# Performance work log

Hardware: AMD Instinct MI355X
Metric: run time of the kernel (lower is better)

## Reference

```python
import jax, jax.numpy as jnp
import numpy as np

NUM_CHANNELS = 256
NUM_HEADS = 4
HEAD_DIM = 64


def setup_inputs() -> dict:
    key = jax.random.key(0)
    k1, k2, k3, k4, k5 = jax.random.split(key, 5)
    C, H, D = NUM_CHANNELS, NUM_HEADS, HEAD_DIM
    x = jax.random.normal(k1, (8, C, 32, 32), dtype=jnp.float32)
    # projection: Linear(C -> H*D*3); stored as (in, out)
    Wp = jax.random.normal(k2, (C, H * D * 3), dtype=jnp.float32) / np.sqrt(C)
    bp = jnp.zeros((H * D * 3,), dtype=jnp.float32)
    # output: Linear(H*D -> C)
    Wo = jax.random.normal(k3, (H * D, C), dtype=jnp.float32) / np.sqrt(H * D)
    bo = jnp.zeros((C,), dtype=jnp.float32)
    return {"x": x, "Wp": Wp, "bp": bp, "Wo": Wo, "bo": bo}


def reference(x, Wp, bp, Wo, bo):
    B, C, Hh, Ww = x.shape
    Nh, Dh = NUM_HEADS, HEAD_DIM
    scale = Dh ** (-0.5)
    # (B, C, H, W) -> (B, N, C)
    xs = x.reshape(B, C, Hh * Ww).transpose(0, 2, 1)
    # QKV projection -> (B, N, heads, 3*head_dim)
    qkv = (xs @ Wp + bp).reshape(B, -1, Nh, 3 * Dh)
    q, k, v = jnp.split(qkv, 3, axis=-1)  # each (B, N, heads, head_dim)
    # NOTE: original forward never applies self.norm, so no GroupNorm here.
    attn = jnp.einsum('bihd,bjhd->bijh', q, k) * scale  # (B, N, N, heads)
    attn = jax.nn.softmax(attn, axis=2)
    res = jnp.einsum('bijh,bjhd->bihd', attn, v)  # (B, N, heads, head_dim)
    res = res.reshape(B, -1, Nh * Dh)
    res = res @ Wo + bo  # (B, N, C)
    out = res + xs
    return out.transpose(0, 2, 1).reshape(B, C, Hh, Ww)
```

## Files before the change

kernel.cpp:

```cpp
#include <hip/hip_runtime.h>

typedef __attribute__((ext_vector_type(8))) short short8;
typedef __attribute__((ext_vector_type(4))) float f32x4;

#define NB 8
#define NC 256
#define NH 4
#define ND 64
#define NN 1024
#define OC3 768

__device__ __forceinline__ unsigned short f2bf(float f) {
  union { float f; unsigned int u; } a;
  a.f = f;
  unsigned int r = a.u + 0x7fffu + ((a.u >> 16) & 1u);
  return (unsigned short)(r >> 16);
}

__device__ __forceinline__ unsigned int pkbf(float lo, float hi) {
  union { float f; unsigned int u; } a, b;
  a.f = lo; b.f = hi;
  return __builtin_amdgcn_perm(b.u + 0x8000u, a.u + 0x8000u, 0x07060302u);
}

typedef const unsigned int __attribute__((address_space(1)))* gp_t;
typedef unsigned int __attribute__((address_space(3)))* lp_t;
__device__ __forceinline__ void glds16(const unsigned short* g, unsigned short* l) {
  __builtin_amdgcn_global_load_lds((gp_t)g, (lp_t)l, 16, 0, 0);
}

__global__ __launch_bounds__(256) void trans_all(
    const float* __restrict__ x, const float* __restrict__ Wp,
    const float* __restrict__ Wo, unsigned short* __restrict__ xs,
    unsigned short* __restrict__ WpT, unsigned short* __restrict__ WoT) {
  __shared__ float T[64][65];
  int z = blockIdx.z;
  const float* in; unsigned short* out; int R, S;
  if (z < 8) { in = x + (size_t)z * NC * NN; out = xs + (size_t)z * NC * NN; R = NC; S = NN; }
  else if (z == 8) { if (blockIdx.x >= 12) return; in = Wp; out = WpT; R = NC; S = OC3; }
  else { if (blockIdx.x >= 4) return; in = Wo; out = WoT; R = NC; S = NC; }
  int s0 = blockIdx.x * 64, r0 = blockIdx.y * 64;
  int t = threadIdx.x;
  {
    int ri = t >> 2, sb = t & 3;
    const float* p = in + (size_t)(r0 + ri) * S + s0 + sb * 16;
    float4 v0 = *(const float4*)(p);
    float4 v1 = *(const float4*)(p + 4);
    float4 v2 = *(const float4*)(p + 8);
    float4 v3 = *(const float4*)(p + 12);
    float vv[16] = {v0.x, v0.y, v0.z, v0.w, v1.x, v1.y, v1.z, v1.w,
                    v2.x, v2.y, v2.z, v2.w, v3.x, v3.y, v3.z, v3.w};
#pragma unroll
    for (int e = 0; e < 16; ++e) T[ri][sb * 16 + e] = vv[e];
  }
  __syncthreads();
  {
    int so = t >> 2, rb = t & 3;
    union { unsigned short us[16]; uint4 v[2]; } pk;
#pragma unroll
    for (int e = 0; e < 16; ++e) pk.us[e] = f2bf(T[rb * 16 + e][so]);
    uint4* dst = (uint4*)(out + (size_t)(s0 + so) * R + r0 + rb * 16);
    dst[0] = pk.v[0];
    dst[1] = pk.v[1];
  }
}

__global__ __launch_bounds__(256) void gemm_qkv(
    const unsigned short* __restrict__ xs, const unsigned short* __restrict__ WpT,
    const float* __restrict__ bp,
    unsigned short* __restrict__ Qf, unsigned short* __restrict__ Kf,
    unsigned short* __restrict__ Vf) {
  __shared__ __attribute__((aligned(16))) unsigned short Al[64 * 72];
  __shared__ __attribute__((aligned(16))) unsigned short Bl[64 * 72];
  int nt = blockIdx.x, mt = blockIdx.y;
  int t = threadIdx.x, w = t >> 6, l = t & 63, q = l >> 4, c = l & 15;
  f32x4 acc[4] = {{0, 0, 0, 0}, {0, 0, 0, 0}, {0, 0, 0, 0}, {0, 0, 0, 0}};
  const unsigned short* Arow = xs + (size_t)(mt * 64) * NC;
  const unsigned short* Brow = WpT + (size_t)(nt * 64) * NC;
  for (int k0 = 0; k0 < NC; k0 += 64) {
    __syncthreads();
#pragma unroll
    for (int it = 0; it < 2; ++it) {
      int u = t + it * 256;
      int row = u >> 3, kb = u & 7;
      *(uint4*)&Al[row * 72 + kb * 8] = *(const uint4*)(Arow + (size_t)row * NC + k0 + kb * 8);
      *(uint4*)&Bl[row * 72 + kb * 8] = *(const uint4*)(Brow + (size_t)row * NC + k0 + kb * 8);
    }
    __syncthreads();
#pragma unroll
    for (int ks = 0; ks < 2; ++ks) {
      short8 a = *(const short8*)&Al[(w * 16 + c) * 72 + ks * 32 + q * 8];
#pragma unroll
      for (int ct = 0; ct < 4; ++ct) {
        short8 b = *(const short8*)&Bl[(ct * 16 + c) * 72 + ks * 32 + q * 8];
        acc[ct] = __builtin_amdgcn_mfma_f32_16x16x32_bf16(a, b, acc[ct], 0, 0, 0);
      }
    }
  }
  int o0 = nt * 64;
  int h = o0 / 192, rem = o0 % 192;
  int b = mt >> 4, itl = mt & 15;
  int bh = b * NH + h;
  size_t rbase = (size_t)bh * 65536;
#pragma unroll
  for (int ct = 0; ct < 4; ++ct) {
    float bias = bp[o0 + ct * 16 + c];
#pragma unroll
    for (int r = 0; r < 4; ++r) acc[ct][r] += bias;
  }
  if (rem < 128) {
    unsigned short* dst = (rem == 0) ? Qf : Kf;
    float sc = (rem == 0) ? 0.18033688011112042f : 1.0f;
#pragma unroll
    for (int ct = 0; ct < 4; ++ct) {
      int ks = ct >> 1, qf = (ct & 1) * 2 + (c >> 3), e = c & 7;
      size_t fbase = (rem == 0)
          ? rbase + (size_t)((itl * 4 + w) * 2 + ks) * 512
          : rbase + (size_t)(itl * 8 + ks * 4 + w) * 512;
      size_t off = fbase + (size_t)(qf * 16) * 8 + e;
#pragma unroll
      for (int r = 0; r < 4; ++r)
        dst[off + (q * 4 + r) * 8] = f2bf(acc[ct][r] * sc);
    }
  } else {
    int kv = w >> 1, ql = (w & 1) * 2 + (q >> 1);
#pragma unroll
    for (int ct = 0; ct < 4; ++ct) {
      size_t fbase = rbase + (size_t)(itl * 8 + kv * 4 + ct) * 512 + (ql * 16 + c) * 8
                   + (q & 1) * 4;
      uint2 pk2 = {pkbf(acc[ct][0], acc[ct][1]), pkbf(acc[ct][2], acc[ct][3])};
      *(uint2*)&Vf[fbase] = pk2;
    }
  }
}

__global__ __launch_bounds__(256) void attn(
    const unsigned short* __restrict__ Qf, const unsigned short* __restrict__ Kf,
    const unsigned short* __restrict__ Vf, unsigned short* __restrict__ O) {
  __shared__ __attribute__((aligned(16))) unsigned short Kl[2][4096];
  __shared__ __attribute__((aligned(16))) unsigned short Vl[2][4096];
  __shared__ __attribute__((aligned(16))) unsigned short Pl[4][1024];
  int B = blockIdx.x;
  int bh = (B & 7) + 8 * ((B >> 3) & 3);
  int it = B >> 5;
  int t = threadIdx.x, w = t >> 6, l = t & 63, q = l >> 4, c = l & 15;
  const unsigned short* Qt = Qf + (size_t)bh * 65536 + (size_t)(it * 4 + w) * 1024;
  short8 bq0 = *(const short8*)(Qt + l * 8);
  short8 bq1 = *(const short8*)(Qt + 512 + l * 8);
  const unsigned short* Kt = Kf + (size_t)bh * 65536;
  const unsigned short* Vt = Vf + (size_t)bh * 65536;

#pragma unroll
  for (int m = 0; m < 2; ++m) {
    int ch = (m * 4 + w) * 512;
    glds16(Kt + ch + l * 8, &Kl[0][ch]);
    glds16(Vt + ch + l * 8, &Vl[0][ch]);
  }

  float lsum = 0.f;
  f32x4 oacc[4] = {{0, 0, 0, 0}, {0, 0, 0, 0}, {0, 0, 0, 0}, {0, 0, 0, 0}};
  unsigned short* Pw = &Pl[w][0];
  int p = 0;
  for (int jt = 0; jt < 16; ++jt) {
    __syncthreads();
    if (jt < 15) {
      const unsigned short* ksn = Kt + (size_t)(jt + 1) * 4096;
      const unsigned short* vsn = Vt + (size_t)(jt + 1) * 4096;
#pragma unroll
      for (int m = 0; m < 2; ++m) {
        int ch = (m * 4 + w) * 512;
        glds16(ksn + ch + l * 8, &Kl[p ^ 1][ch]);
        glds16(vsn + ch + l * 8, &Vl[p ^ 1][ch]);
      }
    }
    f32x4 sT[4] = {{0, 0, 0, 0}, {0, 0, 0, 0}, {0, 0, 0, 0}, {0, 0, 0, 0}};
#pragma unroll
    for (int ks = 0; ks < 2; ++ks) {
      short8 bq = ks ? bq1 : bq0;
#pragma unroll
      for (int js = 0; js < 4; ++js) {
        short8 ka = *(const short8*)&Kl[p][(ks * 4 + js) * 512 + l * 8];
        sT[js] = __builtin_amdgcn_mfma_f32_16x16x32_bf16(ka, bq, sT[js], 0, 0, 0);
      }
    }
#pragma unroll
    for (int js = 0; js < 4; ++js) {
      float e0 = __builtin_amdgcn_exp2f(sT[js][0]);
      float e1 = __builtin_amdgcn_exp2f(sT[js][1]);
      float e2 = __builtin_amdgcn_exp2f(sT[js][2]);
      float e3 = __builtin_amdgcn_exp2f(sT[js][3]);
      lsum += (e0 + e1) + (e2 + e3);
      int base = (js >> 1) * 512 + (((js & 1) * 2 + (q >> 1)) * 16 + c) * 8 + (q & 1) * 4;
      *(unsigned int*)&Pw[base] = pkbf(e0, e1);
      *(unsigned int*)&Pw[base + 2] = pkbf(e2, e3);
    }
#pragma unroll
    for (int kv = 0; kv < 2; ++kv) {
      short8 pa = *(const short8*)&Pw[kv * 512 + l * 8];
#pragma unroll
      for (int dt = 0; dt < 4; ++dt) {
        short8 vv = *(const short8*)&Vl[p][(kv * 4 + dt) * 512 + l * 8];
        oacc[dt] = __builtin_amdgcn_mfma_f32_16x16x32_bf16(pa, vv, oacc[dt], 0, 0, 0);
      }
    }
    p ^= 1;
  }
  lsum += __shfl_xor(lsum, 16);
  lsum += __shfl_xor(lsum, 32);
  float invr[4];
#pragma unroll
  for (int r = 0; r < 4; ++r) invr[r] = 1.0f / __shfl(lsum, q * 4 + r, 64);
  int b = bh >> 2, h = bh & 3;
#pragma unroll
  for (int dt = 0; dt < 4; ++dt)
#pragma unroll
    for (int r = 0; r < 4; ++r) {
      int i = it * 64 + w * 16 + q * 4 + r;
      O[((size_t)b * NN + i) * NC + h * ND + dt * 16 + c] = f2bf(oacc[dt][r] * invr[r]);
    }
}

__global__ __launch_bounds__(256) void gemm_out(
    const unsigned short* __restrict__ O, const unsigned short* __restrict__ WoT,
    const float* __restrict__ bo, const float* __restrict__ x,
    float* __restrict__ out) {
  __shared__ __attribute__((aligned(16))) unsigned short Al[64 * 72];
  __shared__ __attribute__((aligned(16))) unsigned short Bl[64 * 72];
  __shared__ float Tl[64 * 65];
  int nt = blockIdx.x, mt = blockIdx.y;
  int t = threadIdx.x, w = t >> 6, l = t & 63, q = l >> 4, c = l & 15;
  f32x4 acc[4] = {{0, 0, 0, 0}, {0, 0, 0, 0}, {0, 0, 0, 0}, {0, 0, 0, 0}};
  const unsigned short* Arow = O + (size_t)(mt * 64) * NC;
  const unsigned short* Brow = WoT + (size_t)(nt * 64) * NC;
  for (int k0 = 0; k0 < NC; k0 += 64) {
    __syncthreads();
#pragma unroll
    for (int it = 0; it < 2; ++it) {
      int u = t + it * 256;
      int row = u >> 3, kb = u & 7;
      *(uint4*)&Al[row * 72 + kb * 8] = *(const uint4*)(Arow + (size_t)row * NC + k0 + kb * 8);
      *(uint4*)&Bl[row * 72 + kb * 8] = *(const uint4*)(Brow + (size_t)row * NC + k0 + kb * 8);
    }
    __syncthreads();
#pragma unroll
    for (int ks = 0; ks < 2; ++ks) {
      short8 a = *(const short8*)&Al[(w * 16 + c) * 72 + ks * 32 + q * 8];
#pragma unroll
      for (int ct = 0; ct < 4; ++ct) {
        short8 b = *(const short8*)&Bl[(ct * 16 + c) * 72 + ks * 32 + q * 8];
        acc[ct] = __builtin_amdgcn_mfma_f32_16x16x32_bf16(a, b, acc[ct], 0, 0, 0);
      }
    }
  }
#pragma unroll
  for (int ct = 0; ct < 4; ++ct) {
    float bias = bo[nt * 64 + ct * 16 + c];
#pragma unroll
    for (int r = 0; r < 4; ++r)
      Tl[(ct * 16 + c) * 65 + w * 16 + q * 4 + r] = acc[ct][r] + bias;
  }
  __syncthreads();
  int b = (mt * 64) >> 10, n0 = (mt * 64) & 1023;
  int cl = t >> 2, nb = t & 3;
  float v[16];
#pragma unroll
  for (int e = 0; e < 16; ++e) v[e] = Tl[cl * 65 + nb * 16 + e];
  size_t base = ((size_t)(b * NC + nt * 64 + cl)) * NN + n0 + nb * 16;
#pragma unroll
  for (int g = 0; g < 4; ++g) {
    float4 xv = *(const float4*)(x + base + g * 4);
    float4 ov;
    ov.x = v[g * 4 + 0] + xv.x;
    ov.y = v[g * 4 + 1] + xv.y;
    ov.z = v[g * 4 + 2] + xv.z;
    ov.w = v[g * 4 + 3] + xv.w;
    *(float4*)(out + base + g * 4) = ov;
  }
}

extern "C" void kernel_launch(void* const* d_in, const int* in_sizes, int n_in,
                              void* d_out, int out_size, void* d_ws, size_t ws_size,
                              hipStream_t stream) {
  const float* x = (const float*)d_in[0];
  const float* Wp = (const float*)d_in[1];
  const float* bp = (const float*)d_in[2];
  const float* Wo = (const float*)d_in[3];
  const float* bo = (const float*)d_in[4];
  float* out = (float*)d_out;
  char* ws = (char*)d_ws;
  unsigned short* xs  = (unsigned short*)(ws);
  unsigned short* WpT = (unsigned short*)(ws + 4194304);
  unsigned short* WoT = (unsigned short*)(ws + 4587520);
  unsigned short* Qfr = (unsigned short*)(ws + 4718592);
  unsigned short* Kfr = (unsigned short*)(ws + 8912896);
  unsigned short* Vfr = (unsigned short*)(ws + 13107200);
  unsigned short* Ob  = (unsigned short*)(ws + 17301504);

  hipLaunchKernelGGL(trans_all, dim3(16, 4, 10), dim3(256), 0, stream,
                     x, Wp, Wo, xs, WpT, WoT);
  hipLaunchKernelGGL(gemm_qkv, dim3(12, 128), dim3(256), 0, stream, xs, WpT, bp,
                     Qfr, Kfr, Vfr);
  hipLaunchKernelGGL(attn, dim3(512), dim3(256), 0, stream, Qfr, Kfr, Vfr, Ob);
  hipLaunchKernelGGL(gemm_out, dim3(4, 128), dim3(256), 0, stream, Ob, WoT, bo, x, out);
}
```

Baseline: 107.0 us.

## Switch attention to 32x32x16 MFMA with register P via permlane32_swap

Attention now uses 32x32x16 bf16 MFMA tiles instead of 16x16x32. Each wave pair splits the key dimension of a 32-query tile, and the partial outputs are reduced through LDS at the end. The softmax probabilities are moved into A-operand layout with permlane32_swap rather than a round-trip through shared memory, which removes the per-iteration P store and load. The QKV projection's Q/K/V fragment layout is rewritten to match. The cost is an extra cross-wave reduction and a synchronisation at the end of the kernel.

```diff
diff --git a/kernel.cpp b/kernel.cpp
--- a/kernel.cpp
+++ b/kernel.cpp
@@ -2,6 +2,8 @@
 
 typedef __attribute__((ext_vector_type(8))) short short8;
 typedef __attribute__((ext_vector_type(4))) float f32x4;
+typedef __attribute__((ext_vector_type(16))) float f32x16;
+typedef __attribute__((ext_vector_type(2))) unsigned int u32x2;
 
 #define NB 8
 #define NC 256
@@ -111,25 +113,22 @@
   if (rem < 128) {
     unsigned short* dst = (rem == 0) ? Qf : Kf;
     float sc = (rem == 0) ? 0.18033688011112042f : 1.0f;
+    int tile32 = itl * 2 + (w >> 1);
+    int lpb = (c >> 3) * 32 + (w & 1) * 16 + q * 4;
+    size_t tb = rbase + (size_t)tile32 * 2048 + (size_t)(c & 7);
+#pragma unroll
+    for (int ct = 0; ct < 4; ++ct)
+#pragma unroll
+      for (int r = 0; r < 4; ++r)
+        dst[tb + (size_t)ct * 512 + (size_t)((lpb + r) * 8)] = f2bf(acc[ct][r] * sc);
+  } else {
 #pragma unroll
     for (int ct = 0; ct < 4; ++ct) {
-      int ks = ct >> 1, qf = (ct & 1) * 2 + (c >> 3), e = c & 7;
-      size_t fbase = (rem == 0)
-          ? rbase + (size_t)((itl * 4 + w) * 2 + ks) * 512
-          : rbase + (size_t)(itl * 8 + ks * 4 + w) * 512;
-      size_t off = fbase + (size_t)(qf * 16) * 8 + e;
-#pragma unroll
-      for (int r = 0; r < 4; ++r)
-        dst[off + (q * 4 + r) * 8] = f2bf(acc[ct][r] * sc);
-    }
-  } else {
-    int kv = w >> 1, ql = (w & 1) * 2 + (q >> 1);
-#pragma unroll
-    for (int ct = 0; ct < 4; ++ct) {
-      size_t fbase = rbase + (size_t)(itl * 8 + kv * 4 + ct) * 512 + (ql * 16 + c) * 8
-                   + (q & 1) * 4;
+      int f = itl * 8 + (ct >> 1) * 4 + w;
+      int lp = (q >> 1) * 32 + (ct & 1) * 16 + c;
+      size_t off = rbase + (size_t)f * 512 + (size_t)(lp * 8 + (q & 1) * 4);
       uint2 pk2 = {pkbf(acc[ct][0], acc[ct][1]), pkbf(acc[ct][2], acc[ct][3])};
-      *(uint2*)&Vf[fbase] = pk2;
+      *(uint2*)&Vf[off] = pk2;
     }
   }
 }
@@ -139,14 +138,15 @@
     const unsigned short* __restrict__ Vf, unsigned short* __restrict__ O) {
   __shared__ __attribute__((aligned(16))) unsigned short Kl[2][4096];
   __shared__ __attribute__((aligned(16))) unsigned short Vl[2][4096];
-  __shared__ __attribute__((aligned(16))) unsigned short Pl[4][1024];
   int B = blockIdx.x;
   int bh = (B & 7) + 8 * ((B >> 3) & 3);
   int it = B >> 5;
-  int t = threadIdx.x, w = t >> 6, l = t & 63, q = l >> 4, c = l & 15;
-  const unsigned short* Qt = Qf + (size_t)bh * 65536 + (size_t)(it * 4 + w) * 1024;
-  short8 bq0 = *(const short8*)(Qt + l * 8);
-  short8 bq1 = *(const short8*)(Qt + 512 + l * 8);
+  int t = threadIdx.x, w = t >> 6, l = t & 63;
+  int jh = w & 1, isub = w >> 1;
+  const unsigned short* Qt = Qf + (size_t)bh * 65536 + (size_t)(it * 2 + isub) * 2048;
+  short8 bq[4];
+#pragma unroll
+  for (int dc = 0; dc < 4; ++dc) bq[dc] = *(const short8*)(Qt + dc * 512 + l * 8);
   const unsigned short* Kt = Kf + (size_t)bh * 65536;
   const unsigned short* Vt = Vf + (size_t)bh * 65536;
 
@@ -158,8 +158,8 @@
   }
 
   float lsum = 0.f;
-  f32x4 oacc[4] = {{0, 0, 0, 0}, {0, 0, 0, 0}, {0, 0, 0, 0}, {0, 0, 0, 0}};
-  unsigned short* Pw = &Pl[w][0];
+  f32x16 oacc0 = {0, 0, 0, 0, 0, 0, 0, 0, 0, 0, 0, 0, 0, 0, 0, 0};
+  f32x16 oacc1 = {0, 0, 0, 0, 0, 0, 0, 0, 0, 0, 0, 0, 0, 0, 0, 0};
   int p = 0;
   for (int jt = 0; jt < 16; ++jt) {
     __syncthreads();
@@ -173,51 +173,67 @@
         glds16(vsn + ch + l * 8, &Vl[p ^ 1][ch]);
       }
     }
-    f32x4 sT[4] = {{0, 0, 0, 0}, {0, 0, 0, 0}, {0, 0, 0, 0}, {0, 0, 0, 0}};
-#pragma unroll
-    for (int ks = 0; ks < 2; ++ks) {
-      short8 bq = ks ? bq1 : bq0;
-#pragma unroll
-      for (int js = 0; js < 4; ++js) {
-        short8 ka = *(const short8*)&Kl[p][(ks * 4 + js) * 512 + l * 8];
-        sT[js] = __builtin_amdgcn_mfma_f32_16x16x32_bf16(ka, bq, sT[js], 0, 0, 0);
-      }
-    }
-#pragma unroll
-    for (int js = 0; js < 4; ++js) {
-      float e0 = __builtin_amdgcn_exp2f(sT[js][0]);
-      float e1 = __builtin_amdgcn_exp2f(sT[js][1]);
-      float e2 = __builtin_amdgcn_exp2f(sT[js][2]);
-      float e3 = __builtin_amdgcn_exp2f(sT[js][3]);
-      lsum += (e0 + e1) + (e2 + e3);
-      int base = (js >> 1) * 512 + (((js & 1) * 2 + (q >> 1)) * 16 + c) * 8 + (q & 1) * 4;
-      *(unsigned int*)&Pw[base] = pkbf(e0, e1);
-      *(unsigned int*)&Pw[base + 2] = pkbf(e2, e3);
-    }
-#pragma unroll
-    for (int kv = 0; kv < 2; ++kv) {
-      short8 pa = *(const short8*)&Pw[kv * 512 + l * 8];
-#pragma unroll
-      for (int dt = 0; dt < 4; ++dt) {
-        short8 vv = *(const short8*)&Vl[p][(kv * 4 + dt) * 512 + l * 8];
-        oacc[dt] = __builtin_amdgcn_mfma_f32_16x16x32_bf16(pa, vv, oacc[dt], 0, 0, 0);
-      }
+    f32x16 sT = {0, 0, 0, 0, 0, 0, 0, 0, 0, 0, 0, 0, 0, 0, 0, 0};
+#pragma unroll
+    for (int dc = 0; dc < 4; ++dc) {
+      short8 ka = *(const short8*)&Kl[p][(jh * 4 + dc) * 512 + l * 8];
+      sT = __builtin_amdgcn_mfma_f32_32x32x16_bf16(ka, bq[dc], sT, 0, 0, 0);
+    }
+    float e_[16];
+#pragma unroll
+    for (int rg = 0; rg < 16; ++rg) {
+      e_[rg] = __builtin_amdgcn_exp2f(sT[rg]);
+      lsum += e_[rg];
+    }
+#pragma unroll
+    for (int kk = 0; kk < 2; ++kk) {
+      unsigned int x1 = pkbf(e_[kk * 8 + 0], e_[kk * 8 + 1]);
+      unsigned int x2 = pkbf(e_[kk * 8 + 2], e_[kk * 8 + 3]);
+      unsigned int y1 = pkbf(e_[kk * 8 + 4], e_[kk * 8 + 5]);
+      unsigned int y2 = pkbf(e_[kk * 8 + 6], e_[kk * 8 + 7]);
+      u32x2 r1 = __builtin_amdgcn_permlane32_swap(x1, y1, false, false);
+      u32x2 r2 = __builtin_amdgcn_permlane32_swap(x2, y2, false, false);
+      union { unsigned int u[4]; short8 s; } pa;
+      pa.u[0] = r1.x; pa.u[1] = r2.x; pa.u[2] = r1.y; pa.u[3] = r2.y;
+      int kc = jh * 2 + kk;
+      short8 v0 = *(const short8*)&Vl[p][kc * 512 + l * 8];
+      short8 v1 = *(const short8*)&Vl[p][(4 + kc) * 512 + l * 8];
+      oacc0 = __builtin_amdgcn_mfma_f32_32x32x16_bf16(pa.s, v0, oacc0, 0, 0, 0);
+      oacc1 = __builtin_amdgcn_mfma_f32_32x32x16_bf16(pa.s, v1, oacc1, 0, 0, 0);
     }
     p ^= 1;
   }
-  lsum += __shfl_xor(lsum, 16);
   lsum += __shfl_xor(lsum, 32);
-  float invr[4];
-#pragma unroll
-  for (int r = 0; r < 4; ++r) invr[r] = 1.0f / __shfl(lsum, q * 4 + r, 64);
-  int b = bh >> 2, h = bh & 3;
-#pragma unroll
-  for (int dt = 0; dt < 4; ++dt)
-#pragma unroll
-    for (int r = 0; r < 4; ++r) {
-      int i = it * 64 + w * 16 + q * 4 + r;
-      O[((size_t)b * NN + i) * NC + h * ND + dt * 16 + c] = f2bf(oacc[dt][r] * invr[r]);
-    }
+  __syncthreads();
+  float* LF = (float*)&Kl[0][0];
+  float* LS = (float*)&Vl[0][0];
+  int pr = w >> 1;
+  if (w & 1) {
+#pragma unroll
+    for (int rg = 0; rg < 16; ++rg) {
+      LF[pr * 2048 + rg * 64 + l] = oacc0[rg];
+      LF[pr * 2048 + 1024 + rg * 64 + l] = oacc1[rg];
+    }
+    LS[pr * 64 + l] = lsum;
+  }
+  __syncthreads();
+  if (!(w & 1)) {
+    lsum += LS[pr * 64 + l];
+    float inv = 1.0f / lsum;
+    int hi = l >> 5, cl = l & 31;
+    int b = bh >> 2, h = bh & 3;
+    int i0 = it * 64 + isub * 32;
+#pragma unroll
+    for (int rg = 0; rg < 16; ++rg) {
+      int ri = (rg & 3) + 8 * (rg >> 2) + 4 * hi;
+      float invr = __shfl(inv, ri, 64);
+      float o0v = oacc0[rg] + LF[pr * 2048 + rg * 64 + l];
+      float o1v = oacc1[rg] + LF[pr * 2048 + 1024 + rg * 64 + l];
+      size_t base = ((size_t)b * NN + (i0 + ri)) * NC + h * ND + cl;
+      O[base] = f2bf(o0v * invr);
+      O[base + 32] = f2bf(o1v * invr);
+    }
+  }
 }
 
 __global__ __launch_bounds__(256) void gemm_out(
```

Result: no change. 105.7 us (-1.3%).
